# Kernel tuning notes

Measured on AMD Instinct MI355X. Metric: run time of the kernel, lower is better.

## Reference

```python
import jax, jax.numpy as jnp
import numpy as np

SCALING_FACTOR = 1.0


def setup_inputs() -> dict:
    key = jax.random.key(0)
    k1, k2, k3 = jax.random.split(key, 3)
    B, N1, N2, DX, DZ, NT, NK = 4, 64, 64, 2, 128, 2048, 2
    x_grid = jax.random.uniform(k1, (B, N1, N2, DX), dtype=jnp.float32)
    z_grid = jax.random.normal(k2, (B, N1, N2, DZ), dtype=jnp.float32)
    xt = jax.random.uniform(k3, (B, NT, DX), dtype=jnp.float32)
    # Replicates torch init: logspace around log10(init_lengthscale), inverse-softplus
    init_ls = np.logspace(np.log10(0.1) - 0.5, np.log10(0.1) + 0.5, NK).astype(np.float32)
    init_ls = np.tile(init_ls[None, :], (DX, 1))  # (dim, num_kernels)
    lengthscale_param = jnp.asarray(np.log(np.expm1(init_ls)))
    return {"x_grid": x_grid, "z_grid": z_grid, "xt": xt, "lengthscale_param": lengthscale_param}


def reference(x_grid, z_grid, xt, lengthscale_param):
    B = x_grid.shape[0]
    xg = x_grid.reshape(B, -1, x_grid.shape[-1])   # (b, ng, dx)
    zg = z_grid.reshape(B, -1, z_grid.shape[-1])   # (b, ng, dz)
    ls = 1e-5 + jax.nn.softplus(lengthscale_param)  # (dx, nk)
    # EQ/RBF weights: (b, nt, ng, nk)
    diff = (xt[:, :, None, :, None] - xg[:, None, :, :, None]) / ls[None, None, None]
    weights = jnp.exp(-0.5 * jnp.sum(diff * diff, axis=3))
    # weighted smoothing: per-kernel matmul weights @ z_grid, then interleave as (dz nk)
    out = jnp.einsum('btgk,bgz->btzk', weights, zg) / SCALING_FACTOR  # (b, nt, dz, nk)
    return out.reshape(B, xt.shape[1], -1)  # (b, nt, dz*nk), nk fastest like 'b nt (dz nk)'
```

## Files before the change

### kernel.cpp

```cpp
#include <hip/hip_runtime.h>
#include <hip/hip_bf16.h>
#include <cmath>

#define B_   4
#define NT_  2048
#define G_   4096
#define DZ_  128

typedef __attribute__((ext_vector_type(8))) short bf16x8;
typedef __attribute__((ext_vector_type(4))) float f32x4;

__device__ __forceinline__ float softplus_f(float x) {
    return fmaxf(x, 0.0f) + log1pf(expf(-fabsf(x)));
}

__global__ __launch_bounds__(256, 1)
void transpose_z(const float* __restrict__ z, unsigned short* __restrict__ zt)
{
    __shared__ unsigned short tile[64][66];
    const int bx = blockIdx.x;
    const int zti = bx & 1;
    const int gt  = (bx >> 1) & 63;
    const int b   = bx >> 7;
    const int g0 = gt * 64, z0 = zti * 64;
    const int tid = threadIdx.x;
    const int zl = tid & 63, gl = tid >> 6;
    #pragma unroll
    for (int i = 0; i < 16; ++i) {
        const int g = gl + i * 4;
        const float v = z[(size_t)(b * G_ + g0 + g) * DZ_ + z0 + zl];
        unsigned int u = __float_as_uint(v);
        u = u + 0x7FFFu + ((u >> 16) & 1u);
        tile[g][zl] = (unsigned short)(u >> 16);
    }
    __syncthreads();
    const int gp = (tid & 31) * 2, zi = tid >> 5;
    const int c  = (g0 + gp) >> 5, gi = gp & 31;
    #pragma unroll
    for (int i = 0; i < 8; ++i) {
        const int zz = zi + i * 8;
        const unsigned int lo = tile[gp][zz], hi = tile[gp + 1][zz];
        *(unsigned int*)(zt + ((size_t)(b * 128 + c) * 128 + z0 + zz) * 32 + gi)
            = lo | (hi << 16);
    }
}

__global__ __launch_bounds__(512, 2)
void setconv_main(const float* __restrict__ xt,
                  const float* __restrict__ xg,
                  const float* __restrict__ lsp,
                  const unsigned short* __restrict__ Zt,
                  float* __restrict__ out)
{
    __shared__ __align__(16) float red[16384];

    const int bx = blockIdx.x;
    const int b  = bx & 3;
    const int tt = bx >> 2;
    const int tid  = threadIdx.x;
    const int w    = tid >> 6;
    const int ts   = w >> 2;
    const int p    = w & 3;
    const int lane = tid & 63;
    const int quad = lane >> 4;
    const int l15  = lane & 15;
    const int t0   = tt * 32;

    float c00, c01, c10, c11;
    {
        const float h = -0.72134752f;
        float ls;
        ls = 1e-5f + softplus_f(lsp[0]); c00 = h / (ls * ls);
        ls = 1e-5f + softplus_f(lsp[1]); c01 = h / (ls * ls);
        ls = 1e-5f + softplus_f(lsp[2]); c10 = h / (ls * ls);
        ls = 1e-5f + softplus_f(lsp[3]); c11 = h / (ls * ls);
    }

    const float xt0 = xt[(size_t)(b * NT_ + t0 + ts * 16 + l15) * 2 + 0];
    const float xt1 = xt[(size_t)(b * NT_ + t0 + ts * 16 + l15) * 2 + 1];

    f32x4 acc[2][8];
    #pragma unroll
    for (int k = 0; k < 2; ++k)
        #pragma unroll
        for (int n = 0; n < 8; ++n) acc[k][n] = (f32x4)0.0f;

    const unsigned short* zb = Zt + (size_t)(b * 128 + p * 32) * 4096
                               + l15 * 32 + quad * 8;
    const float* xgq = xg + (size_t)(b * G_ + p * 1024 + quad * 8) * 2;

    bf16x8 bzA[8], bzB[8];

    #pragma unroll
    for (int nt = 0; nt < 8; ++nt)
        bzA[nt] = *(const bf16x8*)(zb + nt * 512);

    #define CHUNK(CH, BZC, BZN)                                                \
    {                                                                          \
        const int ch_ = (CH);                                                  \
        const float* xp = xgq + ch_ * 64;                                      \
        const float4 xv0 = *(const float4*)(xp + 0);                           \
        const float4 xv1 = *(const float4*)(xp + 4);                           \
        const float4 xv2 = *(const float4*)(xp + 8);                           \
        const float4 xv3 = *(const float4*)(xp + 12);                          \
        float gx[8], gy[8];                                                    \
        gx[0]=xv0.x; gy[0]=xv0.y; gx[1]=xv0.z; gy[1]=xv0.w;                    \
        gx[2]=xv1.x; gy[2]=xv1.y; gx[3]=xv1.z; gy[3]=xv1.w;                    \
        gx[4]=xv2.x; gy[4]=xv2.y; gx[5]=xv2.z; gy[5]=xv2.w;                    \
        gx[6]=xv3.x; gy[6]=xv3.y; gx[7]=xv3.z; gy[7]=xv3.w;                    \
        union { bf16x8 v; unsigned int u[4]; } a0, a1;                         \
        {                                                                      \
            unsigned int w0b[8], w1b[8];                                       \
            _Pragma("unroll")                                                  \
            for (int j = 0; j < 8; ++j) {                                      \
                const float d0 = xt0 - gx[j];                                  \
                const float d1 = xt1 - gy[j];                                  \
                const float q0 = d0 * d0;                                      \
                const float q1 = d1 * d1;                                      \
                const float e0 = fmaf(q1, c10, q0 * c00);                      \
                const float e1 = fmaf(q1, c11, q0 * c01);                      \
                w0b[j] = __float_as_uint(__builtin_amdgcn_exp2f(e0));          \
                w1b[j] = __float_as_uint(__builtin_amdgcn_exp2f(e1));          \
            }                                                                  \
            _Pragma("unroll")                                                  \
            for (int h = 0; h < 4; ++h) {                                      \
                a0.u[h] = __builtin_amdgcn_perm(w0b[2*h+1], w0b[2*h], 0x07060302u); \
                a1.u[h] = __builtin_amdgcn_perm(w1b[2*h+1], w1b[2*h], 0x07060302u); \
            }                                                                  \
        }                                                                      \
              \
        if (ch_ < 31) {                                                        \
            const unsigned short* zc = zb + (size_t)(ch_ + 1) * 4096;          \
            _Pragma("unroll")                                                  \
            for (int nt = 0; nt < 8; ++nt)                                     \
                BZN[nt] = *(const bf16x8*)(zc + nt * 512);                     \
        }                                                                      \
        _Pragma("unroll")                                                      \
        for (int nt = 0; nt < 8; ++nt) {                                       \
            acc[0][nt] = __builtin_amdgcn_mfma_f32_16x16x32_bf16(a0.v, BZC[nt], acc[0][nt], 0, 0, 0); \
            acc[1][nt] = __builtin_amdgcn_mfma_f32_16x16x32_bf16(a1.v, BZC[nt], acc[1][nt], 0, 0, 0); \
        }                                                                      \
    }

    for (int q = 0; q < 16; ++q) {
        CHUNK(2 * q,     bzA, bzB);
        CHUNK(2 * q + 1, bzB, bzA);
    }
    #undef CHUNK

    #define RED_W(slot) { \
        float* bp = &red[(slot) * 4096 + lane * 4]; \
        _Pragma("unroll") \
        for (int k = 0; k < 2; ++k) \
            _Pragma("unroll") \
            for (int n = 0; n < 8; ++n) \
                *(f32x4*)(bp + (k * 8 + n) * 256) = acc[k][n]; }
    #define RED_A(slot) { \
        const float* bp = &red[(slot) * 4096 + lane * 4]; \
        _Pragma("unroll") \
        for (int k = 0; k < 2; ++k) \
            _Pragma("unroll") \
            for (int n = 0; n < 8; ++n) \
                acc[k][n] += *(const f32x4*)(bp + (k * 8 + n) * 256); }

    __syncthreads();
    if (p >= 2) RED_W(ts * 2 + (p - 2));
    __syncthreads();
    if (p < 2) RED_A(ts * 2 + p);
    __syncthreads();
    if (p == 1) RED_W(ts);
    __syncthreads();
    if (p == 0) {
        RED_A(ts);
        const int tr = t0 + ts * 16 + quad * 4;
        #pragma unroll
        for (int nt = 0; nt < 8; ++nt) {
            float* ob = out + (size_t)(b * NT_ + tr) * (DZ_ * 2) + (nt * 16 + l15) * 2;
            #pragma unroll
            for (int r = 0; r < 4; ++r)
                *(float2*)(ob + (size_t)r * (DZ_ * 2)) =
                    make_float2(acc[0][nt][r], acc[1][nt][r]);
        }
    }
    #undef RED_W
    #undef RED_A
}

extern "C" void kernel_launch(void* const* d_in, const int* in_sizes, int n_in,
                              void* d_out, int out_size, void* d_ws, size_t ws_size,
                              hipStream_t stream)
{
    const float* x_grid = (const float*)d_in[0];
    const float* z_grid = (const float*)d_in[1];
    const float* xt     = (const float*)d_in[2];
    const float* lsp    = (const float*)d_in[3];
    float* out = (float*)d_out;
    unsigned short* Zt = (unsigned short*)d_ws;

    hipLaunchKernelGGL(transpose_z, dim3(512), dim3(256), 0, stream, z_grid, Zt);
    hipLaunchKernelGGL(setconv_main, dim3(256), dim3(512), 0, stream,
                       xt, x_grid, lsp, Zt, out);
}
```

Before: 112.4 us.

## Split the two kernel lengthscales across separate waves with 1024-thread blocks

Doubles the block to 1024 threads so that each wave handles a single lengthscale kernel (kk) rather than both. Per-wave accumulators drop from 16 to 8 MFMA tiles, and the explicit double-buffered Z prefetch is replaced by a simple loop that loads Z each chunk. This is meant to cut register pressure and raise occupancy. In exchange, each wave recomputes the distance terms and loads Z and xg twice (once per kernel). The output stores also become scalar rather than float2 pairs, and the reduction slots and launch bounds are adjusted to match.

```diff
diff --git a/kernel.cpp b/kernel.cpp
--- a/kernel.cpp
+++ b/kernel.cpp
@@ -45,7 +45,7 @@
     }
 }
 
-__global__ __launch_bounds__(512, 2)
+__global__ __launch_bounds__(1024, 4)
 void setconv_main(const float* __restrict__ xt,
                   const float* __restrict__ xg,
                   const float* __restrict__ lsp,
@@ -59,127 +59,97 @@
     const int tt = bx >> 2;
     const int tid  = threadIdx.x;
     const int w    = tid >> 6;
-    const int ts   = w >> 2;
     const int p    = w & 3;
+    const int kk   = (w >> 2) & 1;
+    const int ts   = w >> 3;
     const int lane = tid & 63;
     const int quad = lane >> 4;
     const int l15  = lane & 15;
     const int t0   = tt * 32;
 
-    float c00, c01, c10, c11;
+    float c0, c1;
     {
         const float h = -0.72134752f;
         float ls;
-        ls = 1e-5f + softplus_f(lsp[0]); c00 = h / (ls * ls);
-        ls = 1e-5f + softplus_f(lsp[1]); c01 = h / (ls * ls);
-        ls = 1e-5f + softplus_f(lsp[2]); c10 = h / (ls * ls);
-        ls = 1e-5f + softplus_f(lsp[3]); c11 = h / (ls * ls);
+        ls = 1e-5f + softplus_f(lsp[2 * 0 + kk]); c0 = h / (ls * ls);
+        ls = 1e-5f + softplus_f(lsp[2 * 1 + kk]); c1 = h / (ls * ls);
     }
 
     const float xt0 = xt[(size_t)(b * NT_ + t0 + ts * 16 + l15) * 2 + 0];
     const float xt1 = xt[(size_t)(b * NT_ + t0 + ts * 16 + l15) * 2 + 1];
 
-    f32x4 acc[2][8];
+    f32x4 acc[8];
     #pragma unroll
-    for (int k = 0; k < 2; ++k)
-        #pragma unroll
-        for (int n = 0; n < 8; ++n) acc[k][n] = (f32x4)0.0f;
+    for (int n = 0; n < 8; ++n) acc[n] = (f32x4)0.0f;
 
     const unsigned short* zb = Zt + (size_t)(b * 128 + p * 32) * 4096
                                + l15 * 32 + quad * 8;
     const float* xgq = xg + (size_t)(b * G_ + p * 1024 + quad * 8) * 2;
 
-    bf16x8 bzA[8], bzB[8];
-
-    #pragma unroll
-    for (int nt = 0; nt < 8; ++nt)
-        bzA[nt] = *(const bf16x8*)(zb + nt * 512);
-
-    #define CHUNK(CH, BZC, BZN)                                                \
-    {                                                                          \
-        const int ch_ = (CH);                                                  \
-        const float* xp = xgq + ch_ * 64;                                      \
-        const float4 xv0 = *(const float4*)(xp + 0);                           \
-        const float4 xv1 = *(const float4*)(xp + 4);                           \
-        const float4 xv2 = *(const float4*)(xp + 8);                           \
-        const float4 xv3 = *(const float4*)(xp + 12);                          \
-        float gx[8], gy[8];                                                    \
-        gx[0]=xv0.x; gy[0]=xv0.y; gx[1]=xv0.z; gy[1]=xv0.w;                    \
-        gx[2]=xv1.x; gy[2]=xv1.y; gx[3]=xv1.z; gy[3]=xv1.w;                    \
-        gx[4]=xv2.x; gy[4]=xv2.y; gx[5]=xv2.z; gy[5]=xv2.w;                    \
-        gx[6]=xv3.x; gy[6]=xv3.y; gx[7]=xv3.z; gy[7]=xv3.w;                    \
-        union { bf16x8 v; unsigned int u[4]; } a0, a1;                         \
-        {                                                                      \
-            unsigned int w0b[8], w1b[8];                                       \
-            _Pragma("unroll")                                                  \
-            for (int j = 0; j < 8; ++j) {                                      \
-                const float d0 = xt0 - gx[j];                                  \
-                const float d1 = xt1 - gy[j];                                  \
-                const float q0 = d0 * d0;                                      \
-                const float q1 = d1 * d1;                                      \
-                const float e0 = fmaf(q1, c10, q0 * c00);                      \
-                const float e1 = fmaf(q1, c11, q0 * c01);                      \
-                w0b[j] = __float_as_uint(__builtin_amdgcn_exp2f(e0));          \
-                w1b[j] = __float_as_uint(__builtin_amdgcn_exp2f(e1));          \
-            }                                                                  \
-            _Pragma("unroll")                                                  \
-            for (int h = 0; h < 4; ++h) {                                      \
-                a0.u[h] = __builtin_amdgcn_perm(w0b[2*h+1], w0b[2*h], 0x07060302u); \
-                a1.u[h] = __builtin_amdgcn_perm(w1b[2*h+1], w1b[2*h], 0x07060302u); \
-            }                                                                  \
-        }                                                                      \
-              \
-        if (ch_ < 31) {                                                        \
-            const unsigned short* zc = zb + (size_t)(ch_ + 1) * 4096;          \
-            _Pragma("unroll")                                                  \
-            for (int nt = 0; nt < 8; ++nt)                                     \
-                BZN[nt] = *(const bf16x8*)(zc + nt * 512);                     \
-        }                                                                      \
-        _Pragma("unroll")                                                      \
-        for (int nt = 0; nt < 8; ++nt) {                                       \
-            acc[0][nt] = __builtin_amdgcn_mfma_f32_16x16x32_bf16(a0.v, BZC[nt], acc[0][nt], 0, 0, 0); \
-            acc[1][nt] = __builtin_amdgcn_mfma_f32_16x16x32_bf16(a1.v, BZC[nt], acc[1][nt], 0, 0, 0); \
-        }                                                                      \
+    for (int ch = 0; ch < 32; ++ch) {
+        const float* xp = xgq + ch * 64;
+        const float4 xv0 = *(const float4*)(xp + 0);
+        const float4 xv1 = *(const float4*)(xp + 4);
+        const float4 xv2 = *(const float4*)(xp + 8);
+        const float4 xv3 = *(const float4*)(xp + 12);
+        bf16x8 bz[8];
+        const unsigned short* zc = zb + (size_t)ch * 4096;
+        #pragma unroll
+        for (int nt = 0; nt < 8; ++nt)
+            bz[nt] = *(const bf16x8*)(zc + nt * 512);
+        float gx[8], gy[8];
+        gx[0]=xv0.x; gy[0]=xv0.y; gx[1]=xv0.z; gy[1]=xv0.w;
+        gx[2]=xv1.x; gy[2]=xv1.y; gx[3]=xv1.z; gy[3]=xv1.w;
+        gx[4]=xv2.x; gy[4]=xv2.y; gx[5]=xv2.z; gy[5]=xv2.w;
+        gx[6]=xv3.x; gy[6]=xv3.y; gx[7]=xv3.z; gy[7]=xv3.w;
+        union { bf16x8 v; unsigned int u[4]; } a;
+        unsigned int wb[8];
+        #pragma unroll
+        for (int j = 0; j < 8; ++j) {
+            const float d0 = xt0 - gx[j];
+            const float d1 = xt1 - gy[j];
+            const float e  = fmaf(d1 * d1, c1, (d0 * d0) * c0);
+            wb[j] = __float_as_uint(__builtin_amdgcn_exp2f(e));
+        }
+        #pragma unroll
+        for (int h = 0; h < 4; ++h)
+            a.u[h] = __builtin_amdgcn_perm(wb[2*h+1], wb[2*h], 0x07060302u);
+        #pragma unroll
+        for (int nt = 0; nt < 8; ++nt)
+            acc[nt] = __builtin_amdgcn_mfma_f32_16x16x32_bf16(a.v, bz[nt], acc[nt], 0, 0, 0);
     }
 
-    for (int q = 0; q < 16; ++q) {
-        CHUNK(2 * q,     bzA, bzB);
-        CHUNK(2 * q + 1, bzB, bzA);
-    }
-    #undef CHUNK
-
+    const int sg = (ts * 2 + kk) * 2;
     #define RED_W(slot) { \
-        float* bp = &red[(slot) * 4096 + lane * 4]; \
+        float* bp = &red[(slot) * 2048 + lane * 4]; \
         _Pragma("unroll") \
-        for (int k = 0; k < 2; ++k) \
-            _Pragma("unroll") \
-            for (int n = 0; n < 8; ++n) \
-                *(f32x4*)(bp + (k * 8 + n) * 256) = acc[k][n]; }
+        for (int n = 0; n < 8; ++n) \
+            *(f32x4*)(bp + n * 256) = acc[n]; }
     #define RED_A(slot) { \
-        const float* bp = &red[(slot) * 4096 + lane * 4]; \
+        const float* bp = &red[(slot) * 2048 + lane * 4]; \
         _Pragma("unroll") \
-        for (int k = 0; k < 2; ++k) \
-            _Pragma("unroll") \
-            for (int n = 0; n < 8; ++n) \
-                acc[k][n] += *(const f32x4*)(bp + (k * 8 + n) * 256); }
+        for (int n = 0; n < 8; ++n) \
+            acc[n] += *(const f32x4*)(bp + n * 256); }
 
     __syncthreads();
-    if (p >= 2) RED_W(ts * 2 + (p - 2));
+    if (p == 2) RED_W(sg);
+    if (p == 3) RED_W(sg + 1);
     __syncthreads();
-    if (p < 2) RED_A(ts * 2 + p);
+    if (p == 0) RED_A(sg);
+    if (p == 1) RED_A(sg + 1);
     __syncthreads();
-    if (p == 1) RED_W(ts);
+    if (p == 1) RED_W(sg);
     __syncthreads();
     if (p == 0) {
-        RED_A(ts);
+        RED_A(sg);
         const int tr = t0 + ts * 16 + quad * 4;
         #pragma unroll
         for (int nt = 0; nt < 8; ++nt) {
-            float* ob = out + (size_t)(b * NT_ + tr) * (DZ_ * 2) + (nt * 16 + l15) * 2;
+            float* ob = out + (size_t)(b * NT_ + tr) * (DZ_ * 2)
+                        + (nt * 16 + l15) * 2 + kk;
             #pragma unroll
             for (int r = 0; r < 4; ++r)
-                *(float2*)(ob + (size_t)r * (DZ_ * 2)) =
-                    make_float2(acc[0][nt][r], acc[1][nt][r]);
+                ob[(size_t)r * (DZ_ * 2)] = acc[nt][r];
         }
     }
     #undef RED_W
@@ -198,6 +168,6 @@
     unsigned short* Zt = (unsigned short*)d_ws;
 
     hipLaunchKernelGGL(transpose_z, dim3(512), dim3(256), 0, stream, z_grid, Zt);
-    hipLaunchKernelGGL(setconv_main, dim3(256), dim3(512), 0, stream,
+    hipLaunchKernelGGL(setconv_main, dim3(256), dim3(1024), 0, stream,
                        xt, x_grid, lsp, Zt, out);
 }
```

Measured after the change: 147.2 us. 31.0% more time.
